# Performance work log

Hardware: AMD Instinct MI355X
Metric: run time of the kernel (lower is better)

The kernel has to match this reference:

```python
import jax, jax.numpy as jnp
import numpy as np
import math

D_MODEL = 1024
N_HEADS = 16
HEAD_DIM = D_MODEL // N_HEADS

def setup_inputs() -> dict:
    key = jax.random.key(0)
    k1, k2, k3 = jax.random.split(key, 3)
    B, T = 4, 2048
    x = jax.random.normal(k1, (B, T, D_MODEL), dtype=jnp.float32)
    # weights stored as [in, out]; equivalent to torch Linear weight.T
    w_qkv = jax.random.normal(k2, (D_MODEL, 3 * D_MODEL), dtype=jnp.float32) * (1.0 / math.sqrt(D_MODEL))
    w_proj = jax.random.normal(k3, (D_MODEL, D_MODEL), dtype=jnp.float32) * (1.0 / math.sqrt(D_MODEL))
    return {"x": x, "w_qkv": w_qkv, "w_proj": w_proj}

def reference(x, w_qkv, w_proj):
    B, T, C = x.shape
    qkv = x @ w_qkv  # [B,T,3C]
    q, k, v = jnp.split(qkv, 3, axis=-1)
    # [B,T,C] -> [B,H,T,Dh]
    def to_heads(t):
        return t.reshape(B, T, N_HEADS, HEAD_DIM).transpose(0, 2, 1, 3)
    q, k, v = to_heads(q), to_heads(k), to_heads(v)
    scale = 1.0 / math.sqrt(HEAD_DIM)
    att = jnp.einsum('bhqd,bhkd->bhqk', q, k) * scale  # [B,H,T,T]
    causal = jnp.tril(jnp.ones((T, T), dtype=bool))
    att = jnp.where(causal[None, None], att, -jnp.inf)
    att = jax.nn.softmax(att, axis=-1)
    y = jnp.einsum('bhqk,bhkd->bhqd', att, v)  # [B,H,T,Dh]
    y = y.transpose(0, 2, 1, 3).reshape(B, T, C)
    return y @ w_proj
```

## Files before the change

### kernel.cpp

```cpp
#include <hip/hip_runtime.h>
#include <hip/hip_bf16.h>

typedef __bf16 bf16x8 __attribute__((ext_vector_type(8)));
typedef __bf16 bf16x4 __attribute__((ext_vector_type(4)));
typedef float  f32x4  __attribute__((ext_vector_type(4)));

#define MFMA16(a,b,c) __builtin_amdgcn_mfma_f32_16x16x32_bf16((a),(b),(c),0,0,0)

#define T_SEQ 2048
#define CDIM  1024
#define NH    16
#define DH    64
#define C3    3072
#define QKS   2048

#define GLDS(g, l) __builtin_amdgcn_global_load_lds( \
    (const __attribute__((address_space(1))) void*)(g), \
    (__attribute__((address_space(3))) void*)(l), 16, 0, 0)

__global__ void cast_f32_bf16_kernel(const float* __restrict__ in,
                                     __bf16* __restrict__ out, int n4) {
  int i = blockIdx.x * 256 + threadIdx.x;
  if (i >= n4) return;
  f32x4 v = ((const f32x4*)in)[i];
  bf16x4 o;
  o[0] = (__bf16)v[0]; o[1] = (__bf16)v[1];
  o[2] = (__bf16)v[2]; o[3] = (__bf16)v[3];
  ((bf16x4*)out)[i] = o;
}

__global__ void transpose_cast_kernel(const float* __restrict__ W,
                                      __bf16* __restrict__ WT, int R, int C,
                                      float qscale, int qcols) {
  __shared__ float tile[32][33];
  int c0 = blockIdx.x * 32, r0 = blockIdx.y * 32;
  int tx = threadIdx.x, ty = threadIdx.y;
#pragma unroll
  for (int i = 0; i < 32; i += 8)
    tile[ty + i][tx] = W[(size_t)(r0 + ty + i) * C + c0 + tx];
  __syncthreads();
#pragma unroll
  for (int i = 0; i < 32; i += 8) {
    int c = c0 + ty + i;
    float sc = (c < qcols) ? qscale : 1.0f;
    WT[(size_t)c * R + r0 + tx] = (__bf16)(tile[tx][ty + i] * sc);
  }
}

template <int MODE>
__global__ __launch_bounds__(512, 1)
void gemm256_kernel(const __bf16* __restrict__ A, const __bf16* __restrict__ BT,
                    void* __restrict__ Cout, __bf16* __restrict__ VTp,
                    int K, int nbn) {
  __shared__ __align__(16) __bf16 S[2][2][2][128 * 64];
  const int tid  = threadIdx.x;
  const int lane = tid & 63;
  const int g    = lane >> 4;
  const int l16  = lane & 15;
  const int wave = tid >> 6;
  const int wm   = wave >> 2;
  const int wn   = wave & 3;

  const int nwg = gridDim.x;
  const int sb  = (blockIdx.x & 7) * (nwg >> 3) + (blockIdx.x >> 3);
  const int bn  = sb % nbn;
  const int bm  = sb / nbn;

  const int srow = tid >> 3;
  const int scol = ((tid & 7) << 4) ^ ((srow & 7) << 4);
  const int swz  = (l16 & 7) << 4;

  const __bf16* Abase = A  + (size_t)(bm * 256 + srow) * K + (scol >> 1);
  const __bf16* Bbase = BT + (size_t)(bn * 256 + srow) * K + (scol >> 1);

  f32x4  acc[8][4] = {};
  bf16x8 ar[4][2];
  bf16x8 br[2][2][2];

#define STAGE(BUF, H, K0) do { \
    const __bf16* sp_ = ((H) < 2 ? Abase : Bbase) + (size_t)((H) & 1) * 128 * K + (K0); \
    char* dp_ = (char*)&S[BUF][(H) >> 1][(H) & 1][0] + tid * 16; \
    GLDS(sp_, dp_); \
    GLDS(sp_ + (size_t)64 * K, dp_ + 8192); \
  } while (0)

#define LDA(BUF, MH) do { \
    const char* ab_ = (const char*)&S[BUF][0][wm][0]; \
    _Pragma("unroll") for (int i_ = 0; i_ < 4; ++i_) { \
      const char* rp_ = ab_ + ((MH) * 64 + i_ * 16 + l16) * 128; \
      _Pragma("unroll") for (int kk_ = 0; kk_ < 2; ++kk_) \
        ar[i_][kk_] = *(const bf16x8*)(rp_ + ((kk_ * 64 + g * 16) ^ swz)); \
    } \
  } while (0)

#define LDB(BUF, NHF) do { \
    const char* bb_ = (const char*)&S[BUF][1][wn >> 1][0]; \
    _Pragma("unroll") for (int j_ = 0; j_ < 2; ++j_) { \
      const char* rp_ = bb_ + ((wn & 1) * 64 + ((NHF) * 2 + j_) * 16 + l16) * 128; \
      _Pragma("unroll") for (int kk_ = 0; kk_ < 2; ++kk_) \
        br[NHF][j_][kk_] = *(const bf16x8*)(rp_ + ((kk_ * 64 + g * 16) ^ swz)); \
    } \
  } while (0)

#define MQUAD2(MH) do { \
    __builtin_amdgcn_s_setprio(1); \
    _Pragma("unroll") for (int kk_ = 0; kk_ < 2; ++kk_) \
      _Pragma("unroll") for (int n_ = 0; n_ < 2; ++n_) \
        _Pragma("unroll") for (int i_ = 0; i_ < 4; ++i_) \
          _Pragma("unroll") for (int j_ = 0; j_ < 2; ++j_) \
            acc[(MH) * 4 + i_][n_ * 2 + j_] = \
                MFMA16(ar[i_][kk_], br[n_][j_][kk_], acc[(MH) * 4 + i_][n_ * 2 + j_]); \
    __builtin_amdgcn_s_setprio(0); \
  } while (0)

#define SBAR do { \
    __builtin_amdgcn_sched_barrier(0); \
    __builtin_amdgcn_s_barrier(); \
    __builtin_amdgcn_sched_barrier(0); \
  } while (0)

  STAGE(0, 0, 0); STAGE(0, 1, 0); STAGE(0, 2, 0); STAGE(0, 3, 0);
  STAGE(1, 0, 64); STAGE(1, 2, 64);
  asm volatile("s_waitcnt vmcnt(4)" ::: "memory");
  SBAR;

  const int NIT = K >> 7;
#pragma unroll 1
  for (int it = 0; it < NIT; ++it) {
    const int k1 = (2 * it + 1) << 6;
    const int k2 = (2 * it + 2) << 6;
    const int k3 = (2 * it + 3) << 6;
    const bool stg = (it + 1) < NIT;

    LDA(0, 0); LDB(0, 0); LDB(0, 1);
    STAGE(1, 3, k1); STAGE(1, 1, k1);
    SBAR; MQUAD2(0); SBAR;

    LDA(0, 1);
    if (stg) {
      STAGE(0, 0, k2); STAGE(0, 2, k2);
      asm volatile("s_waitcnt vmcnt(4)" ::: "memory");
    } else {
      asm volatile("s_waitcnt vmcnt(0)" ::: "memory");
    }
    SBAR; MQUAD2(1); SBAR;

    LDA(1, 0); LDB(1, 0); LDB(1, 1);
    if (stg) { STAGE(0, 3, k2); STAGE(0, 1, k2); }
    SBAR; MQUAD2(0); SBAR;

    LDA(1, 1);
    if (stg) {
      STAGE(1, 0, k3); STAGE(1, 2, k3);
      asm volatile("s_waitcnt vmcnt(4)" ::: "memory");
    }
    SBAR; MQUAD2(1); SBAR;
  }

  if (MODE == 0) {
#pragma unroll
    for (int ii = 0; ii < 8; ++ii) {
      const int row0 = bm * 256 + wm * 128 + ii * 16 + g * 4;
#pragma unroll
      for (int jj = 0; jj < 4; ++jj) {
        const int col = bn * 256 + wn * 64 + jj * 16 + l16;
#pragma unroll
        for (int r = 0; r < 4; ++r)
          ((float*)Cout)[(size_t)(row0 + r) * 1024 + col] = acc[ii][jj][r];
      }
    }
  } else if (bn < 8) {
#pragma unroll
    for (int ii = 0; ii < 8; ++ii) {
      const int row0 = bm * 256 + wm * 128 + ii * 16 + g * 4;
#pragma unroll
      for (int jj = 0; jj < 4; ++jj) {
        const int col = bn * 256 + wn * 64 + jj * 16 + l16;
#pragma unroll
        for (int r = 0; r < 4; ++r)
          ((__bf16*)Cout)[(size_t)(row0 + r) * QKS + col] = (__bf16)acc[ii][jj][r];
      }
    }
  } else {
#pragma unroll
    for (int ii = 0; ii < 8; ++ii) {
      const int row0 = bm * 256 + wm * 128 + ii * 16 + g * 4;
      const int b    = row0 >> 11;
      const int t0   = row0 & 2047;
#pragma unroll
      for (int jj = 0; jj < 4; ++jj) {
        const int c = (bn - 8) * 256 + wn * 64 + jj * 16 + l16;
        bf16x4 pb;
#pragma unroll
        for (int r = 0; r < 4; ++r) pb[r] = (__bf16)acc[ii][jj][r];
        *(bf16x4*)(VTp + ((size_t)((b << 10) + c)) * T_SEQ + t0) = pb;
      }
    }
  }
#undef STAGE
#undef LDA
#undef LDB
#undef MQUAD2
#undef SBAR
}

__global__ __launch_bounds__(512, 1)
void gemm2_kernel(const __bf16* __restrict__ A, const __bf16* __restrict__ BT,
                  float* __restrict__ Cout) {
  __shared__ __align__(16) __bf16 S[2][3][128 * 64];
  const int tid  = threadIdx.x;
  const int lane = tid & 63;
  const int g    = lane >> 4;
  const int l16  = lane & 15;
  const int wave = tid >> 6;
  const int wm   = wave >> 2;
  const int wn   = wave & 3;

  const int K = 1024;
  const int sb = (blockIdx.x & 7) * 32 + (blockIdx.x >> 3);
  const int bn = sb & 7;
  const int bm = sb >> 3;

  const int srow = tid >> 3;
  const int scol = ((tid & 7) << 4) ^ ((srow & 7) << 4);
  const int swz  = (l16 & 7) << 4;

  const __bf16* Abase = A  + (size_t)(bm * 256 + srow) * K + (scol >> 1);
  const __bf16* Bbase = BT + (size_t)(bn * 128 + srow) * K + (scol >> 1);

  f32x4  acc[8][2] = {};
  bf16x8 ar[4][2];
  bf16x8 br[2][2];

#define STAGE2(BUF, U, K0) do { \
    const __bf16* sp_ = ((U) < 2 ? Abase + (size_t)(U) * 128 * K : Bbase) + (K0); \
    char* dp_ = (char*)&S[BUF][U][0] + tid * 16; \
    GLDS(sp_, dp_); \
    GLDS(sp_ + (size_t)64 * K, dp_ + 8192); \
  } while (0)

#define LDA2(BUF, MH) do { \
    const char* ab_ = (const char*)&S[BUF][wm][0]; \
    _Pragma("unroll") for (int i_ = 0; i_ < 4; ++i_) { \
      const char* rp_ = ab_ + ((MH) * 64 + i_ * 16 + l16) * 128; \
      _Pragma("unroll") for (int kk_ = 0; kk_ < 2; ++kk_) \
        ar[i_][kk_] = *(const bf16x8*)(rp_ + ((kk_ * 64 + g * 16) ^ swz)); \
    } \
  } while (0)

#define LDB2(BUF) do { \
    const char* bb_ = (const char*)&S[BUF][2][0]; \
    _Pragma("unroll") for (int j_ = 0; j_ < 2; ++j_) { \
      const char* rp_ = bb_ + (wn * 32 + j_ * 16 + l16) * 128; \
      _Pragma("unroll") for (int kk_ = 0; kk_ < 2; ++kk_) \
        br[j_][kk_] = *(const bf16x8*)(rp_ + ((kk_ * 64 + g * 16) ^ swz)); \
    } \
  } while (0)

#define MQ2(MH) do { \
    __builtin_amdgcn_s_setprio(1); \
    _Pragma("unroll") for (int kk_ = 0; kk_ < 2; ++kk_) \
      _Pragma("unroll") for (int i_ = 0; i_ < 4; ++i_) \
        _Pragma("unroll") for (int j_ = 0; j_ < 2; ++j_) \
          acc[(MH) * 4 + i_][j_] = \
              MFMA16(ar[i_][kk_], br[j_][kk_], acc[(MH) * 4 + i_][j_]); \
    __builtin_amdgcn_s_setprio(0); \
  } while (0)

#define SBAR2 do { \
    __builtin_amdgcn_sched_barrier(0); \
    __builtin_amdgcn_s_barrier(); \
    __builtin_amdgcn_sched_barrier(0); \
  } while (0)

  STAGE2(0, 0, 0); STAGE2(0, 1, 0); STAGE2(0, 2, 0);
  STAGE2(1, 0, 64);
  asm volatile("s_waitcnt vmcnt(2)" ::: "memory");
  SBAR2;

  const int NIT = K >> 7;
#pragma unroll 1
  for (int it = 0; it < NIT; ++it) {
    const int k1 = (2 * it + 1) << 6;
    const int k2 = (2 * it + 2) << 6;
    const int k3 = (2 * it + 3) << 6;
    const bool stg = (it + 1) < NIT;

    LDA2(0, 0); LDB2(0);
    STAGE2(1, 1, k1); STAGE2(1, 2, k1);
    SBAR2; MQ2(0); SBAR2;

    LDA2(0, 1);
    if (stg) {
      STAGE2(0, 0, k2);
      asm volatile("s_waitcnt vmcnt(2)" ::: "memory");
    } else {
      asm volatile("s_waitcnt vmcnt(0)" ::: "memory");
    }
    SBAR2; MQ2(1); SBAR2;

    LDA2(1, 0); LDB2(1);
    if (stg) { STAGE2(0, 1, k2); STAGE2(0, 2, k2); }
    SBAR2; MQ2(0); SBAR2;

    LDA2(1, 1);
    if (stg) {
      STAGE2(1, 0, k3);
      asm volatile("s_waitcnt vmcnt(2)" ::: "memory");
    }
    SBAR2; MQ2(1); SBAR2;
  }

#pragma unroll
  for (int ii = 0; ii < 8; ++ii) {
    const int row0 = bm * 256 + wm * 128 + ii * 16 + g * 4;
#pragma unroll
    for (int jj = 0; jj < 2; ++jj) {
      const int col = bn * 128 + wn * 32 + jj * 16 + l16;
#pragma unroll
      for (int r = 0; r < 4; ++r)
        Cout[(size_t)(row0 + r) * 1024 + col] = acc[ii][jj][r];
    }
  }
#undef STAGE2
#undef LDA2
#undef LDB2
#undef MQ2
#undef SBAR2
}

__global__ __launch_bounds__(256)
void attn_kernel(const __bf16* __restrict__ qk, const __bf16* __restrict__ VT,
                 __bf16* __restrict__ y) {
  __shared__ __align__(16) __bf16 Klds[2][64 * 64];
  __shared__ __align__(16) __bf16 Vlds[2][64 * 64];
  __shared__ __align__(16) __bf16 Plds[4][32 * 64];
  const int tid  = threadIdx.x;
  const int lane = tid & 63;
  const int g    = lane >> 4;
  const int l16  = lane & 15;
  const int wave = tid >> 6;

  const int pairid = blockIdx.x >> 6;
  const int bh     = blockIdx.x & 63;
  const int h      = bh & (NH - 1);
  const int b      = bh >> 4;

  const __bf16* Qg = qk + (size_t)b * T_SEQ * QKS + h * DH;
  const __bf16* Kg = Qg + 1024;
  const __bf16* Vt = VT + ((size_t)(b << 10) + h * DH) * T_SEQ;

  const int srow = tid >> 3;
  const int scol = ((tid & 7) * 16) ^ ((srow & 7) << 4);
  const int swz  = (l16 & 7) << 4;

  const float NEG = -3.0e38f;

  bf16x8 ones;
#pragma unroll
  for (int j = 0; j < 8; ++j) ones[j] = (__bf16)1.0f;

  char* Pw = (char*)&Plds[wave][0];

#pragma unroll 1
  for (int ph = 0; ph < 2; ++ph) {
    const int qt    = ph ? (15 - pairid) : pairid;
    const int qbase = qt * 128 + wave * 32;

    bf16x8 qf[2][2];
#pragma unroll
    for (int qg = 0; qg < 2; ++qg)
#pragma unroll
      for (int kk = 0; kk < 2; ++kk)
        qf[qg][kk] = *(const bf16x8*)(Qg + (size_t)(qbase + qg * 16 + l16) * QKS + kk * 32 + g * 8);

    f32x4 o[2][4] = {};
    f32x4 o_l[2]  = {};

    const int nkb = 2 * qt + 2;
    {
      const __bf16* ksrc = Kg + (size_t)srow * QKS + (scol >> 1);
      GLDS(ksrc, (char*)&Klds[0][0] + tid * 16);
      GLDS(ksrc + (size_t)32 * QKS, (char*)&Klds[0][0] + 4096 + tid * 16);
      const __bf16* vsrc = Vt + (size_t)srow * T_SEQ + (scol >> 1);
      GLDS(vsrc, (char*)&Vlds[0][0] + tid * 16);
      GLDS(vsrc + (size_t)32 * T_SEQ, (char*)&Vlds[0][0] + 4096 + tid * 16);
    }
    __syncthreads();

    const __bf16* kstage = Kg + (size_t)(64 + srow) * QKS + (scol >> 1);
    const __bf16* vstage = Vt + (size_t)srow * T_SEQ + 64 + (scol >> 1);

#pragma unroll 1
    for (int kb = 0; kb < nkb; ++kb) {
      const int cur = kb & 1;
      if (kb + 1 < nkb) {
        GLDS(kstage, (char*)&Klds[cur ^ 1][0] + tid * 16);
        GLDS(kstage + (size_t)32 * QKS, (char*)&Klds[cur ^ 1][0] + 4096 + tid * 16);
        GLDS(vstage, (char*)&Vlds[cur ^ 1][0] + tid * 16);
        GLDS(vstage + (size_t)32 * T_SEQ, (char*)&Vlds[cur ^ 1][0] + 4096 + tid * 16);
        kstage += (size_t)64 * QKS;
        vstage += 64;
      }

      f32x4 s[2][4] = {};
      const char* Kb = (const char*)&Klds[cur][0];
#pragma unroll
      for (int kk = 0; kk < 2; ++kk) {
#pragma unroll
        for (int st = 0; st < 4; ++st) {
          const char* rowp = Kb + (st * 16 + l16) * 128;
          bf16x8 kf = *(const bf16x8*)(rowp + ((kk * 64 + g * 16) ^ swz));
          s[0][st] = MFMA16(kf, qf[0][kk], s[0][st]);
          s[1][st] = MFMA16(kf, qf[1][kk], s[1][st]);
        }
      }
      if (kb >= 2 * qt) {
        const int kvbase = (kb - 2 * qt) * 64;
#pragma unroll
        for (int qg = 0; qg < 2; ++qg) {
          const int qloc = wave * 32 + qg * 16 + l16;
#pragma unroll
          for (int st = 0; st < 4; ++st)
#pragma unroll
            for (int r = 0; r < 4; ++r)
              if (kvbase + st * 16 + g * 4 + r > qloc) s[qg][st][r] = NEG;
        }
      }
#pragma unroll
      for (int qg = 0; qg < 2; ++qg) {
        char* Pr = Pw + (qg * 16 + l16) * 128;
#pragma unroll
        for (int st = 0; st < 4; ++st) {
          bf16x4 pb;
#pragma unroll
          for (int r = 0; r < 4; ++r)
            pb[r] = (__bf16)__builtin_amdgcn_exp2f(s[qg][st][r]);
          *(bf16x4*)(Pr + ((st * 32 + g * 8) ^ swz)) = pb;
        }
      }

      const char* Vb = (const char*)&Vlds[cur][0];
#pragma unroll
      for (int hf = 0; hf < 2; ++hf) {
        bf16x8 pf0 = *(const bf16x8*)(Pw + (l16)       * 128 + ((hf * 64 + g * 16) ^ swz));
        bf16x8 pf1 = *(const bf16x8*)(Pw + (16 + l16)  * 128 + ((hf * 64 + g * 16) ^ swz));
        o_l[0] = MFMA16(ones, pf0, o_l[0]);
        o_l[1] = MFMA16(ones, pf1, o_l[1]);
#pragma unroll
        for (int dt = 0; dt < 4; ++dt) {
          bf16x8 vf = *(const bf16x8*)(Vb + (dt * 16 + l16) * 128 + ((hf * 64 + g * 16) ^ swz));
          o[0][dt] = MFMA16(vf, pf0, o[0][dt]);
          o[1][dt] = MFMA16(vf, pf1, o[1][dt]);
        }
      }
      __syncthreads();
    }

#pragma unroll
    for (int qg = 0; qg < 2; ++qg) {
      const float inv_l = 1.0f / o_l[qg][0];
      const int qrow = qbase + qg * 16 + l16;
#pragma unroll
      for (int dt = 0; dt < 4; ++dt)
#pragma unroll
        for (int r = 0; r < 4; ++r)
          y[((size_t)b * T_SEQ + qrow) * CDIM + h * DH + dt * 16 + g * 4 + r] =
              (__bf16)(o[qg][dt][r] * inv_l);
    }
  }
}

extern "C" void kernel_launch(void* const* d_in, const int* in_sizes, int n_in,
                              void* d_out, int out_size, void* d_ws, size_t ws_size,
                              hipStream_t stream) {
  const float* x      = (const float*)d_in[0];
  const float* w_qkv  = (const float*)d_in[1];
  const float* w_proj = (const float*)d_in[2];
  float* out = (float*)d_out;

  __bf16* xb     = (__bf16*)d_ws;
  __bf16* wqkvT  = xb + 8388608;
  __bf16* wprojT = wqkvT + 3145728;
  __bf16* qk     = wprojT + 1048576;
  __bf16* VT     = qk + 16777216;
  __bf16* yb     = VT + 8388608;

  const float SCF = 0.125f * 1.44269504088896340736f;

  cast_f32_bf16_kernel<<<8192, 256, 0, stream>>>(x, xb, 2097152);
  transpose_cast_kernel<<<dim3(96, 32), dim3(32, 8), 0, stream>>>(w_qkv, wqkvT, 1024, 3072, SCF, 1024);
  transpose_cast_kernel<<<dim3(32, 32), dim3(32, 8), 0, stream>>>(w_proj, wprojT, 1024, 1024, 1.0f, 0);
  gemm256_kernel<1><<<384, 512, 0, stream>>>(xb, wqkvT, (void*)qk, VT, 1024, 12);
  attn_kernel<<<512, 256, 0, stream>>>(qk, VT, yb);
  gemm2_kernel<<<256, 512, 0, stream>>>(yb, wprojT, out);
}
```

Before: 164.9 us.

## Replace 256x256 QKV GEMM with 128x128 tiles at two workgroups per CU

```diff
diff --git a/kernel.cpp b/kernel.cpp
--- a/kernel.cpp
+++ b/kernel.cpp
@@ -47,69 +47,68 @@
   }
 }
 
-template <int MODE>
-__global__ __launch_bounds__(512, 1)
-void gemm256_kernel(const __bf16* __restrict__ A, const __bf16* __restrict__ BT,
-                    void* __restrict__ Cout, __bf16* __restrict__ VTp,
-                    int K, int nbn) {
-  __shared__ __align__(16) __bf16 S[2][2][2][128 * 64];
+__global__ __launch_bounds__(256, 2)
+void gemm1_kernel(const __bf16* __restrict__ A, const __bf16* __restrict__ BT,
+                  __bf16* __restrict__ qkp, __bf16* __restrict__ VTp) {
+  __shared__ __align__(16) __bf16 S[2][2][128 * 64];
+  const int K = 1024;
   const int tid  = threadIdx.x;
   const int lane = tid & 63;
   const int g    = lane >> 4;
   const int l16  = lane & 15;
   const int wave = tid >> 6;
-  const int wm   = wave >> 2;
-  const int wn   = wave & 3;
-
-  const int nwg = gridDim.x;
-  const int sb  = (blockIdx.x & 7) * (nwg >> 3) + (blockIdx.x >> 3);
-  const int bn  = sb % nbn;
-  const int bm  = sb / nbn;
+  const int wm   = wave >> 1;
+  const int wn   = wave & 1;
+
+  const int sb = (blockIdx.x & 7) * 192 + (blockIdx.x >> 3);
+  const int bn = sb % 24;
+  const int bm = sb / 24;
 
   const int srow = tid >> 3;
   const int scol = ((tid & 7) << 4) ^ ((srow & 7) << 4);
   const int swz  = (l16 & 7) << 4;
 
-  const __bf16* Abase = A  + (size_t)(bm * 256 + srow) * K + (scol >> 1);
-  const __bf16* Bbase = BT + (size_t)(bn * 256 + srow) * K + (scol >> 1);
-
-  f32x4  acc[8][4] = {};
-  bf16x8 ar[4][2];
-  bf16x8 br[2][2][2];
-
-#define STAGE(BUF, H, K0) do { \
-    const __bf16* sp_ = ((H) < 2 ? Abase : Bbase) + (size_t)((H) & 1) * 128 * K + (K0); \
-    char* dp_ = (char*)&S[BUF][(H) >> 1][(H) & 1][0] + tid * 16; \
-    GLDS(sp_, dp_); \
-    GLDS(sp_ + (size_t)64 * K, dp_ + 8192); \
-  } while (0)
-
-#define LDA(BUF, MH) do { \
-    const char* ab_ = (const char*)&S[BUF][0][wm][0]; \
-    _Pragma("unroll") for (int i_ = 0; i_ < 4; ++i_) { \
-      const char* rp_ = ab_ + ((MH) * 64 + i_ * 16 + l16) * 128; \
+  const __bf16* Abase = A  + (size_t)(bm * 128 + srow) * K + (scol >> 1);
+  const __bf16* Bbase = BT + (size_t)(bn * 128 + srow) * K + (scol >> 1);
+
+  f32x4  acc[4][4] = {};
+  bf16x8 ar[2][2];
+  bf16x8 br[4][2];
+
+#define STAGE_A(BUF, K0) do { \
+    _Pragma("unroll") for (int u_ = 0; u_ < 4; ++u_) \
+      GLDS(Abase + (size_t)u_ * 32 * K + (K0), (char*)&S[BUF][0][0] + u_ * 4096 + tid * 16); \
+  } while (0)
+#define STAGE_B(BUF, K0) do { \
+    _Pragma("unroll") for (int u_ = 0; u_ < 4; ++u_) \
+      GLDS(Bbase + (size_t)u_ * 32 * K + (K0), (char*)&S[BUF][1][0] + u_ * 4096 + tid * 16); \
+  } while (0)
+
+#define LDA(BUF, IH) do { \
+    const char* ab_ = (const char*)&S[BUF][0][0]; \
+    _Pragma("unroll") for (int i_ = 0; i_ < 2; ++i_) { \
+      const char* rp_ = ab_ + (wm * 64 + (IH) * 32 + i_ * 16 + l16) * 128; \
       _Pragma("unroll") for (int kk_ = 0; kk_ < 2; ++kk_) \
         ar[i_][kk_] = *(const bf16x8*)(rp_ + ((kk_ * 64 + g * 16) ^ swz)); \
     } \
   } while (0)
 
-#define LDB(BUF, NHF) do { \
-    const char* bb_ = (const char*)&S[BUF][1][wn >> 1][0]; \
-    _Pragma("unroll") for (int j_ = 0; j_ < 2; ++j_) { \
-      const char* rp_ = bb_ + ((wn & 1) * 64 + ((NHF) * 2 + j_) * 16 + l16) * 128; \
+#define LDB(BUF) do { \
+    const char* bb_ = (const char*)&S[BUF][1][0]; \
+    _Pragma("unroll") for (int j_ = 0; j_ < 4; ++j_) { \
+      const char* rp_ = bb_ + (wn * 64 + j_ * 16 + l16) * 128; \
       _Pragma("unroll") for (int kk_ = 0; kk_ < 2; ++kk_) \
-        br[NHF][j_][kk_] = *(const bf16x8*)(rp_ + ((kk_ * 64 + g * 16) ^ swz)); \
+        br[j_][kk_] = *(const bf16x8*)(rp_ + ((kk_ * 64 + g * 16) ^ swz)); \
     } \
   } while (0)
 
-#define MQUAD2(MH) do { \
+#define MQ(IH) do { \
     __builtin_amdgcn_s_setprio(1); \
     _Pragma("unroll") for (int kk_ = 0; kk_ < 2; ++kk_) \
-      _Pragma("unroll") for (int n_ = 0; n_ < 2; ++n_) \
-        _Pragma("unroll") for (int i_ = 0; i_ < 4; ++i_) \
-          _Pragma("unroll") for (int j_ = 0; j_ < 2; ++j_) \
-            acc[(MH) * 4 + i_][n_ * 2 + j_] = \
-                MFMA16(ar[i_][kk_], br[n_][j_][kk_], acc[(MH) * 4 + i_][n_ * 2 + j_]); \
+      _Pragma("unroll") for (int i_ = 0; i_ < 2; ++i_) \
+        _Pragma("unroll") for (int j_ = 0; j_ < 4; ++j_) \
+          acc[(IH) * 2 + i_][j_] = \
+              MFMA16(ar[i_][kk_], br[j_][kk_], acc[(IH) * 2 + i_][j_]); \
     __builtin_amdgcn_s_setprio(0); \
   } while (0)
 
@@ -119,88 +118,67 @@
     __builtin_amdgcn_sched_barrier(0); \
   } while (0)
 
-  STAGE(0, 0, 0); STAGE(0, 1, 0); STAGE(0, 2, 0); STAGE(0, 3, 0);
-  STAGE(1, 0, 64); STAGE(1, 2, 64);
-  asm volatile("s_waitcnt vmcnt(4)" ::: "memory");
+  STAGE_A(0, 0); STAGE_B(0, 0);
+  asm volatile("s_waitcnt vmcnt(0)" ::: "memory");
   SBAR;
 
   const int NIT = K >> 7;
 #pragma unroll 1
   for (int it = 0; it < NIT; ++it) {
-    const int k1 = (2 * it + 1) << 6;
-    const int k2 = (2 * it + 2) << 6;
-    const int k3 = (2 * it + 3) << 6;
+    const int kt1 = (2 * it + 1) << 6;
+    const int kt2 = (2 * it + 2) << 6;
     const bool stg = (it + 1) < NIT;
 
-    LDA(0, 0); LDB(0, 0); LDB(0, 1);
-    STAGE(1, 3, k1); STAGE(1, 1, k1);
-    SBAR; MQUAD2(0); SBAR;
+    LDA(0, 0); LDB(0);
+    STAGE_A(1, kt1); STAGE_B(1, kt1);
+    SBAR; MQ(0); SBAR;
 
     LDA(0, 1);
-    if (stg) {
-      STAGE(0, 0, k2); STAGE(0, 2, k2);
-      asm volatile("s_waitcnt vmcnt(4)" ::: "memory");
-    } else {
-      asm volatile("s_waitcnt vmcnt(0)" ::: "memory");
-    }
-    SBAR; MQUAD2(1); SBAR;
-
-    LDA(1, 0); LDB(1, 0); LDB(1, 1);
-    if (stg) { STAGE(0, 3, k2); STAGE(0, 1, k2); }
-    SBAR; MQUAD2(0); SBAR;
+    asm volatile("s_waitcnt vmcnt(0)" ::: "memory");
+    SBAR; MQ(1); SBAR;
+
+    LDA(1, 0); LDB(1);
+    if (stg) { STAGE_A(0, kt2); STAGE_B(0, kt2); }
+    SBAR; MQ(0); SBAR;
 
     LDA(1, 1);
-    if (stg) {
-      STAGE(1, 0, k3); STAGE(1, 2, k3);
-      asm volatile("s_waitcnt vmcnt(4)" ::: "memory");
-    }
-    SBAR; MQUAD2(1); SBAR;
-  }
-
-  if (MODE == 0) {
-#pragma unroll
-    for (int ii = 0; ii < 8; ++ii) {
-      const int row0 = bm * 256 + wm * 128 + ii * 16 + g * 4;
+    asm volatile("s_waitcnt vmcnt(0)" ::: "memory");
+    SBAR; MQ(1); SBAR;
+  }
+
+  if (bn < 16) {
+#pragma unroll
+    for (int a = 0; a < 4; ++a) {
+      const int row0 = bm * 128 + wm * 64 + a * 16 + g * 4;
 #pragma unroll
       for (int jj = 0; jj < 4; ++jj) {
-        const int col = bn * 256 + wn * 64 + jj * 16 + l16;
+        const int col = bn * 128 + wn * 64 + jj * 16 + l16;
 #pragma unroll
         for (int r = 0; r < 4; ++r)
-          ((float*)Cout)[(size_t)(row0 + r) * 1024 + col] = acc[ii][jj][r];
-      }
-    }
-  } else if (bn < 8) {
-#pragma unroll
-    for (int ii = 0; ii < 8; ++ii) {
-      const int row0 = bm * 256 + wm * 128 + ii * 16 + g * 4;
-#pragma unroll
-      for (int jj = 0; jj < 4; ++jj) {
-        const int col = bn * 256 + wn * 64 + jj * 16 + l16;
-#pragma unroll
-        for (int r = 0; r < 4; ++r)
-          ((__bf16*)Cout)[(size_t)(row0 + r) * QKS + col] = (__bf16)acc[ii][jj][r];
+          qkp[(size_t)(row0 + r) * QKS + col] = (__bf16)acc[a][jj][r];
       }
     }
   } else {
 #pragma unroll
-    for (int ii = 0; ii < 8; ++ii) {
-      const int row0 = bm * 256 + wm * 128 + ii * 16 + g * 4;
+    for (int a = 0; a < 4; ++a) {
+      const int row0 = bm * 128 + wm * 64 + a * 16 + g * 4;
       const int b    = row0 >> 11;
       const int t0   = row0 & 2047;
 #pragma unroll
       for (int jj = 0; jj < 4; ++jj) {
-        const int c = (bn - 8) * 256 + wn * 64 + jj * 16 + l16;
+        const int c = (bn - 16) * 128 + wn * 64 + jj * 16 + l16;
         bf16x4 pb;
 #pragma unroll
-        for (int r = 0; r < 4; ++r) pb[r] = (__bf16)acc[ii][jj][r];
+        for (int r = 0; r < 4; ++r) pb[r] = (__bf16)acc[a][jj][r];
         *(bf16x4*)(VTp + ((size_t)((b << 10) + c)) * T_SEQ + t0) = pb;
       }
     }
   }
-#undef STAGE
+#undef STAGE_A
+#undef STAGE_B
 #undef LDA
 #undef LDB
-#undef MQUAD2
+#undef MQ
 #undef SBAR
 }
 
@@ -491,7 +469,7 @@
   cast_f32_bf16_kernel<<<8192, 256, 0, stream>>>(x, xb, 2097152);
   transpose_cast_kernel<<<dim3(96, 32), dim3(32, 8), 0, stream>>>(w_qkv, wqkvT, 1024, 3072, SCF, 1024);
   transpose_cast_kernel<<<dim3(32, 32), dim3(32, 8), 0, stream>>>(w_proj, wprojT, 1024, 1024, 1.0f, 0);
-  gemm256_kernel<1><<<384, 512, 0, stream>>>(xb, wqkvT, (void*)qk, VT, 1024, 12);
+  gemm1_kernel<<<1536, 256, 0, stream>>>(xb, wqkvT, qk, VT);
   attn_kernel<<<512, 256, 0, stream>>>(qk, VT, yb);
   gemm2_kernel<<<256, 512, 0, stream>>>(yb, wprojT, out);
 }
```

Result: faster. 153.9 us (-6.7%).
